# Optimization experiments

Measured on AMD Instinct MI355X. Metric: run time of the kernel, lower is better.

The kernel has to match this reference:

```python
import jax, jax.numpy as jnp
import numpy as np

B, CIN, T, H, W = 2, 256, 16, 16, 8
FF, COUT, NHEADS = 512, 256, 8
TEMP = 16.0
BN_EPS = 1e-5


def setup_inputs() -> dict:
    key = jax.random.key(0)
    ks = jax.random.split(key, 6)
    s_in = 1.0 / np.sqrt(CIN)
    s_ff = 1.0 / np.sqrt(FF)
    return {
        "x": jax.random.normal(ks[0], (B, CIN, T, H, W), jnp.float32),
        "WK": jax.random.uniform(ks[1], (FF, CIN), jnp.float32, -s_in, s_in),
        "WQ": jax.random.uniform(ks[2], (FF, CIN), jnp.float32, -s_in, s_in),
        "WV": jax.random.uniform(ks[3], (FF, CIN), jnp.float32, -s_in, s_in),
        "Wo": jax.random.uniform(ks[4], (COUT, FF), jnp.float32, -s_ff, s_ff),
        "bo": jax.random.uniform(ks[5], (COUT,), jnp.float32, -s_ff, s_ff),
        "gamma": jnp.ones((COUT,), jnp.float32),
        "beta": jnp.zeros((COUT,), jnp.float32),
    }


def reference(x, WK, WQ, WV, Wo, bo, gamma, beta):
    N = T * H * W
    xf = x.reshape(B, CIN, N)  # 1x1 conv3d == channel matmul
    dh = FF // NHEADS
    K = jnp.einsum("fc,bcn->bfn", WK, xf).reshape(B, NHEADS, dh, N)
    Q = jnp.einsum("fc,bcn->bfn", WQ, xf).reshape(B, NHEADS, dh, N)
    V = jnp.einsum("fc,bcn->bfn", WV, xf).reshape(B, NHEADS, dh, N)
    # KQ[b,h,i,j] = K_i . Q_j  (i = key token, j = query token, as in torch)
    KQ = jnp.einsum("bhdi,bhdj->bhij", K, Q) / TEMP
    # block-causal mask: token time index t = token_idx // (H*W); tril -> allow i >= j
    t_idx = jnp.arange(N) // (H * W)
    allow = t_idx[:, None] >= t_idx[None, :]  # (N, N)
    KQ = jnp.where(allow[None, None], KQ, -jnp.inf)
    attn = jax.nn.softmax(KQ, axis=3)  # softmax over j (last dim), as in torch
    # out[b,h,d,i] = sum_j V[b,h,d,j] * attn[b,h,i,j]
    Vo = jnp.einsum("bhdj,bhij->bhdi", V, attn).reshape(B, FF, N)
    y = jnp.einsum("of,bfn->bon", Wo, Vo) + bo[None, :, None]
    y = jax.nn.relu(y).reshape(B, COUT, T, H, W)
    out = x + y  # skip: out_dim == in_dim
    # BatchNorm3d (training-mode batch stats, biased var)
    mean = out.mean(axis=(0, 2, 3, 4), keepdims=True)
    var = out.var(axis=(0, 2, 3, 4), keepdims=True)
    norm = (out - mean) * jax.lax.rsqrt(var + BN_EPS)
    return norm * gamma[None, :, None, None, None] + beta[None, :, None, None, None]
```

## Files before the change

### kernel.cpp

```cpp
#include <hip/hip_runtime.h>
#include <math.h>

#define BB_   2
#define CIN_  256
#define NTOK_ 2048
#define FF_   512
#define COUT_ 256
#define NH_   8
#define DH_   64
#define HW_   128
#define BNEPS_ 1e-5f
#define SCALE_LOG2_ 0.09016844005556021f

typedef __attribute__((ext_vector_type(8))) short short8;
typedef __attribute__((ext_vector_type(4))) short bfx4;
typedef __attribute__((ext_vector_type(4))) float f32x4;

#if __has_builtin(__builtin_amdgcn_mfma_f32_16x16x16_bf16)
#define MFMA16(a, b, c) __builtin_amdgcn_mfma_f32_16x16x16_bf16(a, b, c, 0, 0, 0)
#else
#define MFMA16(a, b, c) __builtin_amdgcn_mfma_f32_16x16x16bf16_1k(a, b, c, 0, 0, 0)
#endif

__device__ inline unsigned short f2bf(float f) {
  union { float f; unsigned u; } v; v.f = f;
  unsigned r = (v.u + 0x7FFF + ((v.u >> 16) & 1)) >> 16;
  return (unsigned short)r;
}

__device__ __forceinline__ void dma16(const unsigned short* g, unsigned short* l) {
  __builtin_amdgcn_global_load_lds(
      (const __attribute__((address_space(1))) void*)g,
      (__attribute__((address_space(3))) void*)l, 16, 0, 0);
}

__global__ __launch_bounds__(256, 3) void qkv_kernel(
    const float* __restrict__ x, const float* __restrict__ WK,
    const float* __restrict__ WQ, const float* __restrict__ WV,
    unsigned short* __restrict__ Kb, unsigned short* __restrict__ Qb,
    unsigned short* __restrict__ Vt) {
  __shared__ unsigned short Wsh[128 * 72];
  __shared__ unsigned short Xsh[64 * 72];
  __shared__ float T[64 * 65];
  const int tid = threadIdx.x;
  const int lane = tid & 63, w = tid >> 6;
  const int lx = lane & 15, q = lane >> 4;
  const int wm = w >> 1, wn = w & 1;
  const int n0 = blockIdx.x * 64;
  const int f0 = blockIdx.y * 128;
  const int b = blockIdx.z / 3, which = blockIdx.z % 3;
  const float* Wb = which == 0 ? WK : which == 1 ? WQ : WV;

  const int srow = tid >> 3;
  const int soff = (tid & 7) * 8;
  const float* Wg = Wb + (size_t)(f0 + srow) * CIN_ + soff;
  const int tc = tid >> 4;
  const int tn = (tid & 15) * 4;

  float4 wr[4][2], xr[4];
#pragma unroll
  for (int r = 0; r < 4; ++r) {
    wr[r][0] = *(const float4*)(Wg + (size_t)(32 * r) * CIN_);
    wr[r][1] = *(const float4*)(Wg + (size_t)(32 * r) * CIN_ + 4);
  }
#pragma unroll
  for (int p = 0; p < 4; ++p)
    xr[p] = *(const float4*)(x + (size_t)(b * CIN_ + tc + 16 * p) * NTOK_ + n0 + tn);

  f32x4 acc[4][2];
#pragma unroll
  for (int i = 0; i < 4; ++i)
#pragma unroll
    for (int j = 0; j < 2; ++j) acc[i][j] = (f32x4){0.f, 0.f, 0.f, 0.f};

  for (int kk = 0; kk < 4; ++kk) {
    __syncthreads();
#pragma unroll
    for (int p = 0; p < 4; ++p) {
      const int row = tc + 16 * p;
      T[row * 65 + tn + 0] = xr[p].x; T[row * 65 + tn + 1] = xr[p].y;
      T[row * 65 + tn + 2] = xr[p].z; T[row * 65 + tn + 3] = xr[p].w;
    }
#pragma unroll
    for (int r = 0; r < 4; ++r) {
      unsigned short u[8];
      u[0] = f2bf(wr[r][0].x); u[1] = f2bf(wr[r][0].y);
      u[2] = f2bf(wr[r][0].z); u[3] = f2bf(wr[r][0].w);
      u[4] = f2bf(wr[r][1].x); u[5] = f2bf(wr[r][1].y);
      u[6] = f2bf(wr[r][1].z); u[7] = f2bf(wr[r][1].w);
      *(uint4*)(Wsh + (srow + 32 * r) * 72 + soff) = *(uint4*)u;
    }
    __syncthreads();
#pragma unroll
    for (int p = 0; p < 2; ++p) {
      const int idx = tid + 256 * p;
      const int nl = idx >> 3, c8 = (idx & 7) * 8;
      unsigned short u[8];
#pragma unroll
      for (int i = 0; i < 8; ++i) u[i] = f2bf(T[(c8 + i) * 65 + nl]);
      *(uint4*)(Xsh + nl * 72 + c8) = *(uint4*)u;
    }
    if (kk < 3) {
      const int c0 = (kk + 1) * 64;
#pragma unroll
      for (int r = 0; r < 4; ++r) {
        wr[r][0] = *(const float4*)(Wg + (size_t)(32 * r) * CIN_ + c0);
        wr[r][1] = *(const float4*)(Wg + (size_t)(32 * r) * CIN_ + c0 + 4);
      }
#pragma unroll
      for (int p = 0; p < 4; ++p)
        xr[p] = *(const float4*)(x + (size_t)(b * CIN_ + c0 + tc + 16 * p) * NTOK_ + n0 + tn);
    }
    __syncthreads();
    short8 xF[2][2];
#pragma unroll
    for (int i = 0; i < 2; ++i) {
      xF[i][0] = *(const short8*)(Xsh + (32 * wn + 16 * i + lx) * 72 + q * 8);
      xF[i][1] = *(const short8*)(Xsh + (32 * wn + 16 * i + lx) * 72 + 32 + q * 8);
    }
    if (which < 2) {
#pragma unroll
      for (int i = 0; i < 4; ++i) {
        const short8 w0 = *(const short8*)(Wsh + (64 * wm + 16 * i + lx) * 72 + q * 8);
        const short8 w1 = *(const short8*)(Wsh + (64 * wm + 16 * i + lx) * 72 + 32 + q * 8);
#pragma unroll
        for (int j = 0; j < 2; ++j) {
          acc[i][j] = __builtin_amdgcn_mfma_f32_16x16x32_bf16(w0, xF[j][0], acc[i][j], 0, 0, 0);
          acc[i][j] = __builtin_amdgcn_mfma_f32_16x16x32_bf16(w1, xF[j][1], acc[i][j], 0, 0, 0);
        }
      }
    } else {
#pragma unroll
      for (int jf = 0; jf < 4; ++jf) {
        const short8 w0 = *(const short8*)(Wsh + (64 * wm + 16 * jf + lx) * 72 + q * 8);
        const short8 w1 = *(const short8*)(Wsh + (64 * wm + 16 * jf + lx) * 72 + 32 + q * 8);
#pragma unroll
        for (int i = 0; i < 2; ++i) {
          acc[jf][i] = __builtin_amdgcn_mfma_f32_16x16x32_bf16(xF[i][0], w0, acc[jf][i], 0, 0, 0);
          acc[jf][i] = __builtin_amdgcn_mfma_f32_16x16x32_bf16(xF[i][1], w1, acc[jf][i], 0, 0, 0);
        }
      }
    }
  }

  __syncthreads();

  if (which < 2) {
    const float sc = (which == 0) ? SCALE_LOG2_ : 1.0f;
#pragma unroll
    for (int i = 0; i < 4; ++i)
#pragma unroll
      for (int j = 0; j < 2; ++j) {
        const int row = wm * 64 + 32 * wn + 16 * j + lx;
        const int d0 = 16 * i + 4 * q;
        ushort4 u;
        u.x = f2bf(acc[i][j][0] * sc); u.y = f2bf(acc[i][j][1] * sc);
        u.z = f2bf(acc[i][j][2] * sc); u.w = f2bf(acc[i][j][3] * sc);
        *(ushort4*)(Wsh + row * 72 + d0) = u;
      }
  } else {
#pragma unroll
    for (int jf = 0; jf < 4; ++jf)
#pragma unroll
      for (int i = 0; i < 2; ++i) {
        const int row = wm * 64 + 16 * jf + lx;
        const int nc = 32 * wn + 16 * i + 4 * q;
        ushort4 u;
        u.x = f2bf(acc[jf][i][0]); u.y = f2bf(acc[jf][i][1]);
        u.z = f2bf(acc[jf][i][2]); u.w = f2bf(acc[jf][i][3]);
        *(ushort4*)(Wsh + row * 72 + nc) = u;
      }
  }
  __syncthreads();

  const int h0 = f0 >> 6;
  if (which < 2) {
    unsigned short* Y = (which == 0 ? Kb : Qb);
#pragma unroll
    for (int p = 0; p < 4; ++p) {
      const int idx = tid + 256 * p;
      const int row = idx >> 3;
      const int c = (idx & 7) * 8;
      const uint4 val = *(const uint4*)(Wsh + row * 72 + c);
      *(uint4*)(Y + ((size_t)((b * NH_ + h0 + (row >> 6)) * NTOK_ + n0 + (row & 63))) * DH_ + c) = val;
    }
  } else {
#pragma unroll
    for (int p = 0; p < 4; ++p) {
      const int idx = tid + 256 * p;
      const int row = idx >> 3;
      const int c = (idx & 7) * 8;
      const uint4 val = *(const uint4*)(Wsh + row * 72 + c);
      *(uint4*)(Vt + ((size_t)((b * NH_ + h0 + (row >> 6)) * DH_ + (row & 63))) * NTOK_ + n0 + c) = val;
    }
  }
}

__global__ __launch_bounds__(256, 2) void attn_kernel(
    const unsigned short* __restrict__ Kb, const unsigned short* __restrict__ Qb,
    const unsigned short* __restrict__ Vt, unsigned short* __restrict__ Ob) {
  __shared__ __align__(16) unsigned short Qbuf[2][8192];
  __shared__ __align__(16) unsigned short Vbuf[2][8192];

  const int tid = threadIdx.x;
  const int lane = tid & 63;
  const int w = tid >> 6;
  const int lx = lane & 15;
  const int g = lane >> 4;

  const int bid = blockIdx.x;
  const int xcd = bid & 7;
  const int k = bid >> 3;
  const int bh = xcd * 2 + (k & 1);
  const int u = k >> 1;
  const int iblk = (u < 16) ? (31 - u) : (u - 16);
  const int h = bh & 7, b = bh >> 3;
  const int i0 = iblk * 64;
  const int njt = (iblk >> 1) + 1;

  const size_t bhs = (size_t)b * NH_ + h;
  const unsigned short* Kg = Kb + bhs * (size_t)NTOK_ * DH_ + (size_t)i0 * DH_;
  const unsigned short* Qg = Qb + bhs * (size_t)NTOK_ * DH_;
  const unsigned short* Vg = Vt + bhs * (size_t)DH_ * NTOK_;

  auto stage = [&](int buf, int j0) {
#pragma unroll
    for (int cc = 0; cc < 4; ++cc) {
      const int chunk = 4 * w + cc;
      {
        const int row = chunk * 8 + (lane >> 3);
        const int grp = (lane & 7) ^ (row & 7);
        dma16(Qg + (size_t)(j0 + row) * DH_ + grp * 8, &Qbuf[buf][chunk * 512]);
      }
      {
        const int row = chunk * 4 + (lane >> 4);
        const int grp = (lane & 15) ^ (row & 7);
        dma16(Vg + (size_t)row * NTOK_ + j0 + grp * 8, &Vbuf[buf][chunk * 512]);
      }
    }
  };

  const short8 aK0 = *(const short8*)(Kg + (16 * w + lx) * DH_ + g * 8);
  const short8 aK1 = *(const short8*)(Kg + (16 * w + lx) * DH_ + 32 + g * 8);

  f32x4 o[4];
#pragma unroll
  for (int t = 0; t < 4; ++t) o[t] = (f32x4){0.f, 0.f, 0.f, 0.f};
  float rs = 0.f;

  const int fr0 = ((g ^ (lx & 7)) << 3);
  const int fr1 = (((4 + g) ^ (lx & 7)) << 3);

  stage(0, 0);
  __syncthreads();

  int cur = 0;
  for (int jt = 0; jt < njt; ++jt) {
    if (jt + 1 < njt) stage(cur ^ 1, (jt + 1) * 128);

    const unsigned short* Qs = Qbuf[cur];
    const unsigned short* Vs = Vbuf[cur];

    f32x4 sa[8];
#pragma unroll
    for (int s = 0; s < 8; ++s) {
      const int row = 16 * s + lx;
      const short8 a0 = *(const short8*)(Qs + row * 64 + fr0);
      const short8 a1 = *(const short8*)(Qs + row * 64 + fr1);
      sa[s] = (f32x4){0.f, 0.f, 0.f, 0.f};
      sa[s] = __builtin_amdgcn_mfma_f32_16x16x32_bf16(a0, aK0, sa[s], 0, 0, 0);
      sa[s] = __builtin_amdgcn_mfma_f32_16x16x32_bf16(a1, aK1, sa[s], 0, 0, 0);
    }

#pragma unroll
    for (int s = 0; s < 8; ++s) {
      const float p0 = __builtin_amdgcn_exp2f(sa[s][0]);
      const float p1 = __builtin_amdgcn_exp2f(sa[s][1]);
      const float p2 = __builtin_amdgcn_exp2f(sa[s][2]);
      const float p3 = __builtin_amdgcn_exp2f(sa[s][3]);
      rs += (p0 + p1) + (p2 + p3);
      union { unsigned u[2]; bfx4 v; } pk;
      pk.u[0] = (__builtin_bit_cast(unsigned, p0) >> 16) |
                (__builtin_bit_cast(unsigned, p1) & 0xFFFF0000u);
      pk.u[1] = (__builtin_bit_cast(unsigned, p2) >> 16) |
                (__builtin_bit_cast(unsigned, p3) & 0xFFFF0000u);
      const int jgrp = 2 * s + (g >> 1);
      const int joff = (g & 1) << 2;
#pragma unroll
      for (int t = 0; t < 4; ++t) {
        const int row = 16 * t + lx;
        const bfx4 va = *(const bfx4*)(Vs + row * 128 +
                                       ((jgrp ^ (row & 7)) << 3) + joff);
        o[t] = MFMA16(va, pk.v, o[t]);
      }
    }

    __syncthreads();
    cur ^= 1;
  }

  rs += __shfl_xor(rs, 16);
  rs += __shfl_xor(rs, 32);
  const float invl = 1.0f / rs;
  const int n = i0 + 16 * w + lx;
#pragma unroll
  for (int t = 0; t < 4; ++t) {
    ushort4 uo;
    uo.x = f2bf(o[t][0] * invl); uo.y = f2bf(o[t][1] * invl);
    uo.z = f2bf(o[t][2] * invl); uo.w = f2bf(o[t][3] * invl);
    *(ushort4*)(Ob + ((size_t)(b * NTOK_ + n)) * FF_ + h * 64 + 16 * t + 4 * g) = uo;
  }
}

__global__ __launch_bounds__(256, 2) void proj_kernel(
    const unsigned short* __restrict__ Ob, const float* __restrict__ Wo,
    const float* __restrict__ bo, const float* __restrict__ x,
    float* __restrict__ pre) {
  __shared__ unsigned short Osh[32 * 72];
  __shared__ unsigned short Wsh[64 * 72];
  const int tid = threadIdx.x;
  const int lane = tid & 63, w = tid >> 6;
  const int lx = lane & 15, q = lane >> 4;
  const int n0 = blockIdx.x * 32;
  const int o0 = blockIdx.y * 64;
  const int b = blockIdx.z;

  const int srow = tid >> 3;
  const int soff = (tid & 7) * 8;
  const unsigned short* Og = Ob + ((size_t)(b * NTOK_ + n0 + srow)) * FF_ + soff;
  const float* Wg = Wo + (size_t)(o0 + srow) * FF_ + soff;

  uint4 orr;
  float4 wrr[2][2];
  orr = *(const uint4*)(Og);
#pragma unroll
  for (int r = 0; r < 2; ++r) {
    wrr[r][0] = *(const float4*)(Wg + (size_t)(32 * r) * FF_);
    wrr[r][1] = *(const float4*)(Wg + (size_t)(32 * r) * FF_ + 4);
  }

  f32x4 acc[2];
#pragma unroll
  for (int i = 0; i < 2; ++i) acc[i] = (f32x4){0.f, 0.f, 0.f, 0.f};

  for (int kk = 0; kk < 8; ++kk) {
    __syncthreads();
    *(uint4*)(Osh + srow * 72 + soff) = orr;
#pragma unroll
    for (int r = 0; r < 2; ++r) {
      unsigned short u[8];
      u[0] = f2bf(wrr[r][0].x); u[1] = f2bf(wrr[r][0].y);
      u[2] = f2bf(wrr[r][0].z); u[3] = f2bf(wrr[r][0].w);
      u[4] = f2bf(wrr[r][1].x); u[5] = f2bf(wrr[r][1].y);
      u[6] = f2bf(wrr[r][1].z); u[7] = f2bf(wrr[r][1].w);
      *(uint4*)(Wsh + (srow + 32 * r) * 72 + soff) = *(uint4*)u;
    }
    if (kk < 7) {
      const int c0 = (kk + 1) * 64;
      orr = *(const uint4*)(Og + c0);
#pragma unroll
      for (int r = 0; r < 2; ++r) {
        wrr[r][0] = *(const float4*)(Wg + (size_t)(32 * r) * FF_ + c0);
        wrr[r][1] = *(const float4*)(Wg + (size_t)(32 * r) * FF_ + c0 + 4);
      }
    }
    __syncthreads();
    short8 aF[2][2], bF[2];
#pragma unroll
    for (int i = 0; i < 2; ++i) {
      aF[i][0] = *(const short8*)(Osh + (16 * i + lx) * 72 + q * 8);
      aF[i][1] = *(const short8*)(Osh + (16 * i + lx) * 72 + 32 + q * 8);
    }
    bF[0] = *(const short8*)(Wsh + (16 * w + lx) * 72 + q * 8);
    bF[1] = *(const short8*)(Wsh + (16 * w + lx) * 72 + 32 + q * 8);
#pragma unroll
    for (int i = 0; i < 2; ++i) {
      acc[i] = __builtin_amdgcn_mfma_f32_16x16x32_bf16(aF[i][0], bF[0], acc[i], 0, 0, 0);
      acc[i] = __builtin_amdgcn_mfma_f32_16x16x32_bf16(aF[i][1], bF[1], acc[i], 0, 0, 0);
    }
  }

  const int o = o0 + 16 * w + lx;
  const float bias = bo[o];
#pragma unroll
  for (int i = 0; i < 2; ++i) {
    const int n = n0 + 16 * i + 4 * q;
    const float4 xv = *(const float4*)(x + ((size_t)(b * CIN_ + o)) * NTOK_ + n);
    float4 v;
    v.x = fmaxf(acc[i][0] + bias, 0.f) + xv.x;
    v.y = fmaxf(acc[i][1] + bias, 0.f) + xv.y;
    v.z = fmaxf(acc[i][2] + bias, 0.f) + xv.z;
    v.w = fmaxf(acc[i][3] + bias, 0.f) + xv.w;
    *(float4*)(pre + ((size_t)(b * COUT_ + o)) * NTOK_ + n) = v;
  }
}

__global__ __launch_bounds__(512) void bn_kernel(
    float* __restrict__ out, const float* __restrict__ gamma,
    const float* __restrict__ beta) {
  __shared__ float red[16];
  const int c = blockIdx.x;
  const int tid = threadIdx.x;
  const int lane = tid & 63, w = tid >> 6;

  float4 v[2];
  float s = 0.f, s2 = 0.f;
#pragma unroll
  for (int b = 0; b < BB_; ++b) {
    float* base = out + ((size_t)(b * COUT_ + c)) * NTOK_;
    const float4 t = *(const float4*)(base + 4 * tid);
    v[b] = t;
    s += t.x + t.y + t.z + t.w;
    s2 += t.x * t.x + t.y * t.y + t.z * t.z + t.w * t.w;
  }
#pragma unroll
  for (int off = 32; off >= 1; off >>= 1) {
    s += __shfl_xor(s, off);
    s2 += __shfl_xor(s2, off);
  }
  if (lane == 0) { red[w] = s; red[8 + w] = s2; }
  __syncthreads();
  float S = 0.f, S2 = 0.f;
#pragma unroll
  for (int i = 0; i < 8; ++i) { S += red[i]; S2 += red[8 + i]; }
  const float inv = 1.0f / (float)(BB_ * NTOK_);
  const float mean = S * inv;
  const float var = S2 * inv - mean * mean;
  const float sc = rsqrtf(var + BNEPS_) * gamma[c];
  const float bt = beta[c];
#pragma unroll
  for (int b = 0; b < BB_; ++b) {
    float* base = out + ((size_t)(b * COUT_ + c)) * NTOK_;
    float4 t = v[b];
    t.x = (t.x - mean) * sc + bt;
    t.y = (t.y - mean) * sc + bt;
    t.z = (t.z - mean) * sc + bt;
    t.w = (t.w - mean) * sc + bt;
    *(float4*)(base + 4 * tid) = t;
  }
}

extern "C" void kernel_launch(void* const* d_in, const int* in_sizes, int n_in,
                              void* d_out, int out_size, void* d_ws, size_t ws_size,
                              hipStream_t stream) {
  (void)in_sizes; (void)n_in; (void)out_size; (void)ws_size;
  const float* x = (const float*)d_in[0];
  const float* WK = (const float*)d_in[1];
  const float* WQ = (const float*)d_in[2];
  const float* WV = (const float*)d_in[3];
  const float* Wo = (const float*)d_in[4];
  const float* bo = (const float*)d_in[5];
  const float* gamma = (const float*)d_in[6];
  const float* beta = (const float*)d_in[7];

  char* ws = (char*)d_ws;
  unsigned short* Kb  = (unsigned short*)(ws + 3145728);
  unsigned short* Qb  = (unsigned short*)(ws + 7340032);
  unsigned short* Vt  = (unsigned short*)(ws + 11534336);
  unsigned short* Ob  = (unsigned short*)(ws + 15728640);
  float* out = (float*)d_out;

  qkv_kernel<<<dim3(32, 4, 6), 256, 0, stream>>>(x, WK, WQ, WV, Kb, Qb, Vt);
  attn_kernel<<<dim3(512, 1, 1), 256, 0, stream>>>(Kb, Qb, Vt, Ob);
  proj_kernel<<<dim3(64, 4, 2), 256, 0, stream>>>(Ob, Wo, bo, x, out);
  bn_kernel<<<256, 512, 0, stream>>>(out, gamma, beta);
}
```

Measured before the change: 119.6 us.

## Fuse BatchNorm into projection kernel via atomic ticket grid barrier

Merges the projection and BatchNorm kernels into one launch. Each block takes a ticket from a global atomic counter. The first 256 blocks exit after writing the pre-norm output. The last 256 spin until all 512 blocks have finished, then each normalizes one channel. This removes a kernel launch and its inter-kernel gap, but adds a memset launch, a spin-wait, and a dependence on all 512 blocks being resident at once to avoid deadlock.

```diff
diff --git a/kernel.cpp b/kernel.cpp
--- a/kernel.cpp
+++ b/kernel.cpp
@@ -312,12 +312,15 @@
   }
 }
 
-__global__ __launch_bounds__(256, 2) void proj_kernel(
+__global__ __launch_bounds__(256, 2) void proj_bn_kernel(
     const unsigned short* __restrict__ Ob, const float* __restrict__ Wo,
     const float* __restrict__ bo, const float* __restrict__ x,
-    float* __restrict__ pre) {
+    float* __restrict__ out, const float* __restrict__ gamma,
+    const float* __restrict__ beta, unsigned* __restrict__ ctr) {
   __shared__ unsigned short Osh[32 * 72];
   __shared__ unsigned short Wsh[64 * 72];
+  __shared__ float red[8];
+  __shared__ unsigned tksh;
   const int tid = threadIdx.x;
   const int lane = tid & 63, w = tid >> 6;
   const int lx = lane & 15, q = lane >> 4;
@@ -380,63 +383,81 @@
     }
   }
 
-  const int o = o0 + 16 * w + lx;
-  const float bias = bo[o];
-#pragma unroll
-  for (int i = 0; i < 2; ++i) {
-    const int n = n0 + 16 * i + 4 * q;
-    const float4 xv = *(const float4*)(x + ((size_t)(b * CIN_ + o)) * NTOK_ + n);
-    float4 v;
-    v.x = fmaxf(acc[i][0] + bias, 0.f) + xv.x;
-    v.y = fmaxf(acc[i][1] + bias, 0.f) + xv.y;
-    v.z = fmaxf(acc[i][2] + bias, 0.f) + xv.z;
-    v.w = fmaxf(acc[i][3] + bias, 0.f) + xv.w;
-    *(float4*)(pre + ((size_t)(b * COUT_ + o)) * NTOK_ + n) = v;
-  }
-}
-
-__global__ __launch_bounds__(512) void bn_kernel(
-    float* __restrict__ out, const float* __restrict__ gamma,
-    const float* __restrict__ beta) {
-  __shared__ float red[16];
-  const int c = blockIdx.x;
-  const int tid = threadIdx.x;
-  const int lane = tid & 63, w = tid >> 6;
-
-  float4 v[2];
+  {
+    const int o = o0 + 16 * w + lx;
+    const float bias = bo[o];
+#pragma unroll
+    for (int i = 0; i < 2; ++i) {
+      const int n = n0 + 16 * i + 4 * q;
+      const float4 xv = *(const float4*)(x + ((size_t)(b * CIN_ + o)) * NTOK_ + n);
+      float4 v;
+      v.x = fmaxf(acc[i][0] + bias, 0.f) + xv.x;
+      v.y = fmaxf(acc[i][1] + bias, 0.f) + xv.y;
+      v.z = fmaxf(acc[i][2] + bias, 0.f) + xv.z;
+      v.w = fmaxf(acc[i][3] + bias, 0.f) + xv.w;
+      *(float4*)(out + ((size_t)(b * COUT_ + o)) * NTOK_ + n) = v;
+    }
+  }
+
+  __syncthreads();
+  if (tid == 0) {
+    tksh = __hip_atomic_fetch_add(ctr, 1u, __ATOMIC_ACQ_REL,
+                                  __HIP_MEMORY_SCOPE_AGENT);
+  }
+  __syncthreads();
+  const unsigned ticket = tksh;
+  if (ticket < 256) return;
+
+  if (tid == 0) {
+    while (__hip_atomic_load(ctr, __ATOMIC_RELAXED,
+                             __HIP_MEMORY_SCOPE_AGENT) < 512u) {
+      __builtin_amdgcn_s_sleep(4);
+    }
+    (void)__hip_atomic_load(ctr, __ATOMIC_ACQUIRE, __HIP_MEMORY_SCOPE_AGENT);
+  }
+  __syncthreads();
+
+  const int c = (int)ticket - 256;
+
+  float4 v[2][2];
   float s = 0.f, s2 = 0.f;
 #pragma unroll
-  for (int b = 0; b < BB_; ++b) {
-    float* base = out + ((size_t)(b * COUT_ + c)) * NTOK_;
-    const float4 t = *(const float4*)(base + 4 * tid);
-    v[b] = t;
-    s += t.x + t.y + t.z + t.w;
-    s2 += t.x * t.x + t.y * t.y + t.z * t.z + t.w * t.w;
+  for (int bb = 0; bb < BB_; ++bb) {
+    float* base = out + ((size_t)(bb * COUT_ + c)) * NTOK_;
+#pragma unroll
+    for (int p = 0; p < 2; ++p) {
+      const float4 t = *(const float4*)(base + 4 * tid + p * 1024);
+      v[bb][p] = t;
+      s += t.x + t.y + t.z + t.w;
+      s2 += t.x * t.x + t.y * t.y + t.z * t.z + t.w * t.w;
+    }
   }
 #pragma unroll
   for (int off = 32; off >= 1; off >>= 1) {
     s += __shfl_xor(s, off);
     s2 += __shfl_xor(s2, off);
   }
-  if (lane == 0) { red[w] = s; red[8 + w] = s2; }
-  __syncthreads();
-  float S = 0.f, S2 = 0.f;
-#pragma unroll
-  for (int i = 0; i < 8; ++i) { S += red[i]; S2 += red[8 + i]; }
+  if (lane == 0) { red[w] = s; red[4 + w] = s2; }
+  __syncthreads();
+  const float S = red[0] + red[1] + red[2] + red[3];
+  const float S2 = red[4] + red[5] + red[6] + red[7];
   const float inv = 1.0f / (float)(BB_ * NTOK_);
   const float mean = S * inv;
   const float var = S2 * inv - mean * mean;
   const float sc = rsqrtf(var + BNEPS_) * gamma[c];
   const float bt = beta[c];
 #pragma unroll
-  for (int b = 0; b < BB_; ++b) {
-    float* base = out + ((size_t)(b * COUT_ + c)) * NTOK_;
-    float4 t = v[b];
-    t.x = (t.x - mean) * sc + bt;
-    t.y = (t.y - mean) * sc + bt;
-    t.z = (t.z - mean) * sc + bt;
-    t.w = (t.w - mean) * sc + bt;
-    *(float4*)(base + 4 * tid) = t;
+  for (int bb = 0; bb < BB_; ++bb) {
+    float* base = out + ((size_t)(bb * COUT_ + c)) * NTOK_;
+#pragma unroll
+    for (int p = 0; p < 2; ++p) {
+      float4 t = v[bb][p];
+      t.x = (t.x - mean) * sc + bt;
+      t.y = (t.y - mean) * sc + bt;
+      t.z = (t.z - mean) * sc + bt;
+      t.w = (t.w - mean) * sc + bt;
+      *(float4*)(base + 4 * tid + p * 1024) = t;
+    }
   }
 }
 
@@ -458,10 +479,12 @@
   unsigned short* Qb  = (unsigned short*)(ws + 7340032);
   unsigned short* Vt  = (unsigned short*)(ws + 11534336);
   unsigned short* Ob  = (unsigned short*)(ws + 15728640);
+  unsigned* ctr       = (unsigned*)(ws + 19922944);
   float* out = (float*)d_out;
 
+  (void)hipMemsetAsync(ctr, 0, 64, stream);
   qkv_kernel<<<dim3(32, 4, 6), 256, 0, stream>>>(x, WK, WQ, WV, Kb, Qb, Vt);
   attn_kernel<<<dim3(512, 1, 1), 256, 0, stream>>>(Kb, Qb, Vt, Ob);
-  proj_kernel<<<dim3(64, 4, 2), 256, 0, stream>>>(Ob, Wo, bo, x, out);
-  bn_kernel<<<256, 512, 0, stream>>>(out, gamma, beta);
-}
+  proj_bn_kernel<<<dim3(64, 4, 2), 256, 0, stream>>>(Ob, Wo, bo, x, out,
+                                                     gamma, beta, ctr);
+}
```

Measured after the change: 144.9 us. +21.1%, slower.

## Load Q and V fragments directly from global memory in attention kernel

Applied to the files above, without the earlier changes.

Removes the double-buffered LDS staging of Q and V tiles through global_load_lds in the attention kernel. Each wave now reads its MFMA operand fragments straight from global memory, relying on the cache for reuse across the four waves. This drops the per-tile barriers and LDS traffic and lifts the occupancy cap, but each wave issues redundant global loads and loses the prefetch overlap.

```diff
diff --git a/kernel.cpp b/kernel.cpp
--- a/kernel.cpp
+++ b/kernel.cpp
@@ -26,12 +26,6 @@
   union { float f; unsigned u; } v; v.f = f;
   unsigned r = (v.u + 0x7FFF + ((v.u >> 16) & 1)) >> 16;
   return (unsigned short)r;
-}
-
-__device__ __forceinline__ void dma16(const unsigned short* g, unsigned short* l) {
-  __builtin_amdgcn_global_load_lds(
-      (const __attribute__((address_space(1))) void*)g,
-      (__attribute__((address_space(3))) void*)l, 16, 0, 0);
 }
 
 __global__ __launch_bounds__(256, 3) void qkv_kernel(
@@ -196,12 +190,9 @@
   }
 }
 
-__global__ __launch_bounds__(256, 2) void attn_kernel(
+__global__ __launch_bounds__(256) void attn_kernel(
     const unsigned short* __restrict__ Kb, const unsigned short* __restrict__ Qb,
     const unsigned short* __restrict__ Vt, unsigned short* __restrict__ Ob) {
-  __shared__ __align__(16) unsigned short Qbuf[2][8192];
-  __shared__ __align__(16) unsigned short Vbuf[2][8192];
-
   const int tid = threadIdx.x;
   const int lane = tid & 63;
   const int w = tid >> 6;
@@ -223,23 +214,6 @@
   const unsigned short* Qg = Qb + bhs * (size_t)NTOK_ * DH_;
   const unsigned short* Vg = Vt + bhs * (size_t)DH_ * NTOK_;
 
-  auto stage = [&](int buf, int j0) {
-#pragma unroll
-    for (int cc = 0; cc < 4; ++cc) {
-      const int chunk = 4 * w + cc;
-      {
-        const int row = chunk * 8 + (lane >> 3);
-        const int grp = (lane & 7) ^ (row & 7);
-        dma16(Qg + (size_t)(j0 + row) * DH_ + grp * 8, &Qbuf[buf][chunk * 512]);
-      }
-      {
-        const int row = chunk * 4 + (lane >> 4);
-        const int grp = (lane & 15) ^ (row & 7);
-        dma16(Vg + (size_t)row * NTOK_ + j0 + grp * 8, &Vbuf[buf][chunk * 512]);
-      }
-    }
-  };
-
   const short8 aK0 = *(const short8*)(Kg + (16 * w + lx) * DH_ + g * 8);
   const short8 aK1 = *(const short8*)(Kg + (16 * w + lx) * DH_ + 32 + g * 8);
 
@@ -248,25 +222,20 @@
   for (int t = 0; t < 4; ++t) o[t] = (f32x4){0.f, 0.f, 0.f, 0.f};
   float rs = 0.f;
 
-  const int fr0 = ((g ^ (lx & 7)) << 3);
-  const int fr1 = (((4 + g) ^ (lx & 7)) << 3);
-
-  stage(0, 0);
-  __syncthreads();
-
-  int cur = 0;
+  const unsigned short* Vrow0 = Vg + (size_t)(lx) * NTOK_;
+  const unsigned short* Vrow1 = Vg + (size_t)(16 + lx) * NTOK_;
+  const unsigned short* Vrow2 = Vg + (size_t)(32 + lx) * NTOK_;
+  const unsigned short* Vrow3 = Vg + (size_t)(48 + lx) * NTOK_;
+
   for (int jt = 0; jt < njt; ++jt) {
-    if (jt + 1 < njt) stage(cur ^ 1, (jt + 1) * 128);
-
-    const unsigned short* Qs = Qbuf[cur];
-    const unsigned short* Vs = Vbuf[cur];
+    const int j0 = jt * 128;
 
     f32x4 sa[8];
 #pragma unroll
     for (int s = 0; s < 8; ++s) {
-      const int row = 16 * s + lx;
-      const short8 a0 = *(const short8*)(Qs + row * 64 + fr0);
-      const short8 a1 = *(const short8*)(Qs + row * 64 + fr1);
+      const int row = j0 + 16 * s + lx;
+      const short8 a0 = *(const short8*)(Qg + (size_t)row * DH_ + g * 8);
+      const short8 a1 = *(const short8*)(Qg + (size_t)row * DH_ + 32 + g * 8);
       sa[s] = (f32x4){0.f, 0.f, 0.f, 0.f};
       sa[s] = __builtin_amdgcn_mfma_f32_16x16x32_bf16(a0, aK0, sa[s], 0, 0, 0);
       sa[s] = __builtin_amdgcn_mfma_f32_16x16x32_bf16(a1, aK1, sa[s], 0, 0, 0);
@@ -284,19 +253,16 @@
                 (__builtin_bit_cast(unsigned, p1) & 0xFFFF0000u);
       pk.u[1] = (__builtin_bit_cast(unsigned, p2) >> 16) |
                 (__builtin_bit_cast(unsigned, p3) & 0xFFFF0000u);
-      const int jgrp = 2 * s + (g >> 1);
-      const int joff = (g & 1) << 2;
-#pragma unroll
-      for (int t = 0; t < 4; ++t) {
-        const int row = 16 * t + lx;
-        const bfx4 va = *(const bfx4*)(Vs + row * 128 +
-                                       ((jgrp ^ (row & 7)) << 3) + joff);
-        o[t] = MFMA16(va, pk.v, o[t]);
-      }
-    }
-
-    __syncthreads();
-    cur ^= 1;
+      const int jc = j0 + 16 * s + 4 * g;
+      const bfx4 va0 = *(const bfx4*)(Vrow0 + jc);
+      const bfx4 va1 = *(const bfx4*)(Vrow1 + jc);
+      const bfx4 va2 = *(const bfx4*)(Vrow2 + jc);
+      const bfx4 va3 = *(const bfx4*)(Vrow3 + jc);
+      o[0] = MFMA16(va0, pk.v, o[0]);
+      o[1] = MFMA16(va1, pk.v, o[1]);
+      o[2] = MFMA16(va2, pk.v, o[2]);
+      o[3] = MFMA16(va3, pk.v, o[3]);
+    }
   }
 
   rs += __shfl_xor(rs, 16);
```

Measured after the change: 193.2 us. 1.61x slower.

## Split attention key range across two blocks with atomic last-block reduction

Applied to the files above, without the earlier changes.

Each (batch, head, query-block) work item is split into two halves of the j-tile range, doubling the attention grid to 1024 blocks. Each block writes fp32 partial outputs and row sums to workspace, and the second block to finish, detected through an agent-scope atomic counter, adds its partner's partials and normalizes. The counters are zeroed inside the QKV kernel. This is meant to shorten the long causal rows and balance load, and it drops the previous heavy-first XCD-aware block ordering. The cost is extra global traffic for the partials, an atomic per pair, and blocks with little or no work for small iblk.

```diff
diff --git a/kernel.cpp b/kernel.cpp
--- a/kernel.cpp
+++ b/kernel.cpp
@@ -38,11 +38,14 @@
     const float* __restrict__ x, const float* __restrict__ WK,
     const float* __restrict__ WQ, const float* __restrict__ WV,
     unsigned short* __restrict__ Kb, unsigned short* __restrict__ Qb,
-    unsigned short* __restrict__ Vt) {
+    unsigned short* __restrict__ Vt, unsigned* __restrict__ ctr) {
   __shared__ unsigned short Wsh[128 * 72];
   __shared__ unsigned short Xsh[64 * 72];
   __shared__ float T[64 * 65];
   const int tid = threadIdx.x;
+  if (blockIdx.x == 0 && blockIdx.y == 0 && blockIdx.z == 0) {
+    ctr[tid] = 0u; ctr[tid + 256] = 0u;
+  }
   const int lane = tid & 63, w = tid >> 6;
   const int lx = lane & 15, q = lane >> 4;
   const int wm = w >> 1, wn = w & 1;
@@ -198,9 +201,12 @@
 
 __global__ __launch_bounds__(256, 2) void attn_kernel(
     const unsigned short* __restrict__ Kb, const unsigned short* __restrict__ Qb,
-    const unsigned short* __restrict__ Vt, unsigned short* __restrict__ Ob) {
+    const unsigned short* __restrict__ Vt, unsigned short* __restrict__ Ob,
+    float* __restrict__ oPart, float* __restrict__ rsPart,
+    unsigned* __restrict__ ctr) {
   __shared__ __align__(16) unsigned short Qbuf[2][8192];
   __shared__ __align__(16) unsigned short Vbuf[2][8192];
+  __shared__ unsigned tksh;
 
   const int tid = threadIdx.x;
   const int lane = tid & 63;
@@ -209,14 +215,16 @@
   const int g = lane >> 4;
 
   const int bid = blockIdx.x;
-  const int xcd = bid & 7;
-  const int k = bid >> 3;
-  const int bh = xcd * 2 + (k & 1);
-  const int u = k >> 1;
-  const int iblk = (u < 16) ? (31 - u) : (u - 16);
+  const int pid = bid >> 1;
+  const int half = bid & 1;
+  const int bh = pid >> 5;
+  const int iblk = pid & 31;
   const int h = bh & 7, b = bh >> 3;
   const int i0 = iblk * 64;
   const int njt = (iblk >> 1) + 1;
+  const int nh = (njt + 1) >> 1;
+  const int jbeg = half ? nh : 0;
+  const int jend = half ? njt : nh;
 
   const size_t bhs = (size_t)b * NH_ + h;
   const unsigned short* Kg = Kb + bhs * (size_t)NTOK_ * DH_ + (size_t)i0 * DH_;
@@ -240,64 +248,85 @@
     }
   };
 
-  const short8 aK0 = *(const short8*)(Kg + (16 * w + lx) * DH_ + g * 8);
-  const short8 aK1 = *(const short8*)(Kg + (16 * w + lx) * DH_ + 32 + g * 8);
-
   f32x4 o[4];
 #pragma unroll
   for (int t = 0; t < 4; ++t) o[t] = (f32x4){0.f, 0.f, 0.f, 0.f};
   float rs = 0.f;
 
-  const int fr0 = ((g ^ (lx & 7)) << 3);
-  const int fr1 = (((4 + g) ^ (lx & 7)) << 3);
-
-  stage(0, 0);
+  if (jbeg < jend) {
+    const short8 aK0 = *(const short8*)(Kg + (16 * w + lx) * DH_ + g * 8);
+    const short8 aK1 = *(const short8*)(Kg + (16 * w + lx) * DH_ + 32 + g * 8);
+    const int fr0 = ((g ^ (lx & 7)) << 3);
+    const int fr1 = (((4 + g) ^ (lx & 7)) << 3);
+
+    stage(0, jbeg * 128);
+    __syncthreads();
+
+    int cur = 0;
+    for (int jt = jbeg; jt < jend; ++jt) {
+      if (jt + 1 < jend) stage(cur ^ 1, (jt + 1) * 128);
+
+      const unsigned short* Qs = Qbuf[cur];
+      const unsigned short* Vs = Vbuf[cur];
+
+      f32x4 sa[8];
+#pragma unroll
+      for (int s = 0; s < 8; ++s) {
+        const int row = 16 * s + lx;
+        const short8 a0 = *(const short8*)(Qs + row * 64 + fr0);
+        const short8 a1 = *(const short8*)(Qs + row * 64 + fr1);
+        sa[s] = (f32x4){0.f, 0.f, 0.f, 0.f};
+        sa[s] = __builtin_amdgcn_mfma_f32_16x16x32_bf16(a0, aK0, sa[s], 0, 0, 0);
+        sa[s] = __builtin_amdgcn_mfma_f32_16x16x32_bf16(a1, aK1, sa[s], 0, 0, 0);
+      }
+
+#pragma unroll
+      for (int s = 0; s < 8; ++s) {
+        const float p0 = __builtin_amdgcn_exp2f(sa[s][0]);
+        const float p1 = __builtin_amdgcn_exp2f(sa[s][1]);
+        const float p2 = __builtin_amdgcn_exp2f(sa[s][2]);
+        const float p3 = __builtin_amdgcn_exp2f(sa[s][3]);
+        rs += (p0 + p1) + (p2 + p3);
+        union { unsigned u[2]; bfx4 v; } pk;
+        pk.u[0] = (__builtin_bit_cast(unsigned, p0) >> 16) |
+                  (__builtin_bit_cast(unsigned, p1) & 0xFFFF0000u);
+        pk.u[1] = (__builtin_bit_cast(unsigned, p2) >> 16) |
+                  (__builtin_bit_cast(unsigned, p3) & 0xFFFF0000u);
+        const int jgrp = 2 * s + (g >> 1);
+        const int joff = (g & 1) << 2;
+#pragma unroll
+        for (int t = 0; t < 4; ++t) {
+          const int row = 16 * t + lx;
+          const bfx4 va = *(const bfx4*)(Vs + row * 128 +
+                                         ((jgrp ^ (row & 7)) << 3) + joff);
+          o[t] = MFMA16(va, pk.v, o[t]);
+        }
+      }
+
+      __syncthreads();
+      cur ^= 1;
+    }
+  }
+
+#pragma unroll
+  for (int t = 0; t < 4; ++t)
+    *(f32x4*)(oPart + (size_t)bid * 4096 + tid * 16 + t * 4) = o[t];
+  rsPart[(size_t)bid * 256 + tid] = rs;
   __syncthreads();
-
-  int cur = 0;
-  for (int jt = 0; jt < njt; ++jt) {
-    if (jt + 1 < njt) stage(cur ^ 1, (jt + 1) * 128);
-
-    const unsigned short* Qs = Qbuf[cur];
-    const unsigned short* Vs = Vbuf[cur];
-
-    f32x4 sa[8];
-#pragma unroll
-    for (int s = 0; s < 8; ++s) {
-      const int row = 16 * s + lx;
-      const short8 a0 = *(const short8*)(Qs + row * 64 + fr0);
-      const short8 a1 = *(const short8*)(Qs + row * 64 + fr1);
-      sa[s] = (f32x4){0.f, 0.f, 0.f, 0.f};
-      sa[s] = __builtin_amdgcn_mfma_f32_16x16x32_bf16(a0, aK0, sa[s], 0, 0, 0);
-      sa[s] = __builtin_amdgcn_mfma_f32_16x16x32_bf16(a1, aK1, sa[s], 0, 0, 0);
-    }
-
-#pragma unroll
-    for (int s = 0; s < 8; ++s) {
-      const float p0 = __builtin_amdgcn_exp2f(sa[s][0]);
-      const float p1 = __builtin_amdgcn_exp2f(sa[s][1]);
-      const float p2 = __builtin_amdgcn_exp2f(sa[s][2]);
-      const float p3 = __builtin_amdgcn_exp2f(sa[s][3]);
-      rs += (p0 + p1) + (p2 + p3);
-      union { unsigned u[2]; bfx4 v; } pk;
-      pk.u[0] = (__builtin_bit_cast(unsigned, p0) >> 16) |
-                (__builtin_bit_cast(unsigned, p1) & 0xFFFF0000u);
-      pk.u[1] = (__builtin_bit_cast(unsigned, p2) >> 16) |
-                (__builtin_bit_cast(unsigned, p3) & 0xFFFF0000u);
-      const int jgrp = 2 * s + (g >> 1);
-      const int joff = (g & 1) << 2;
-#pragma unroll
-      for (int t = 0; t < 4; ++t) {
-        const int row = 16 * t + lx;
-        const bfx4 va = *(const bfx4*)(Vs + row * 128 +
-                                       ((jgrp ^ (row & 7)) << 3) + joff);
-        o[t] = MFMA16(va, pk.v, o[t]);
-      }
-    }
-
-    __syncthreads();
-    cur ^= 1;
-  }
+  if (tid == 0) {
+    tksh = __hip_atomic_fetch_add(&ctr[pid], 1u, __ATOMIC_ACQ_REL,
+                                  __HIP_MEMORY_SCOPE_AGENT);
+  }
+  __syncthreads();
+  if (tksh == 0) return;
+
+  const int pbid = bid ^ 1;
+#pragma unroll
+  for (int t = 0; t < 4; ++t) {
+    const f32x4 po = *(const f32x4*)(oPart + (size_t)pbid * 4096 + tid * 16 + t * 4);
+    o[t][0] += po[0]; o[t][1] += po[1]; o[t][2] += po[2]; o[t][3] += po[3];
+  }
+  rs += rsPart[(size_t)pbid * 256 + tid];
 
   rs += __shfl_xor(rs, 16);
   rs += __shfl_xor(rs, 32);
@@ -458,10 +487,14 @@
   unsigned short* Qb  = (unsigned short*)(ws + 7340032);
   unsigned short* Vt  = (unsigned short*)(ws + 11534336);
   unsigned short* Ob  = (unsigned short*)(ws + 15728640);
+  float* oPart        = (float*)(ws + 33554432);
+  float* rsPart       = (float*)(ws + 52428800);
+  unsigned* ctr       = (unsigned*)(ws + 54525952);
   float* out = (float*)d_out;
 
-  qkv_kernel<<<dim3(32, 4, 6), 256, 0, stream>>>(x, WK, WQ, WV, Kb, Qb, Vt);
-  attn_kernel<<<dim3(512, 1, 1), 256, 0, stream>>>(Kb, Qb, Vt, Ob);
+  qkv_kernel<<<dim3(32, 4, 6), 256, 0, stream>>>(x, WK, WQ, WV, Kb, Qb, Vt, ctr);
+  attn_kernel<<<dim3(1024, 1, 1), 256, 0, stream>>>(Kb, Qb, Vt, Ob,
+                                                    oPart, rsPart, ctr);
   proj_kernel<<<dim3(64, 4, 2), 256, 0, stream>>>(Ob, Wo, bo, x, out);
   bn_kernel<<<256, 512, 0, stream>>>(out, gamma, beta);
 }
```

New measurement: 155.4 us. 29.9% more time.
